# Kernel tuning notes

Measured on AMD Instinct MI355X. Metric: run time of the kernel, lower is better.

Reference implementation:

```python
import jax, jax.numpy as jnp
import numpy as np

EMB = 512
HEADS = 8

def setup_inputs() -> dict:
    key = jax.random.key(0)
    ks = jax.random.split(key, 9)
    s = 1.0 / np.sqrt(EMB)
    return {
        'x':  jax.random.normal(ks[0], (4, 2048, EMB), dtype=jnp.float32),
        'Wq': jax.random.uniform(ks[1], (EMB, EMB), jnp.float32, -s, s),
        'bq': jax.random.uniform(ks[2], (EMB,), jnp.float32, -s, s),
        'Wk': jax.random.uniform(ks[3], (EMB, EMB), jnp.float32, -s, s),
        'bk': jax.random.uniform(ks[4], (EMB,), jnp.float32, -s, s),
        'Wv': jax.random.uniform(ks[5], (EMB, EMB), jnp.float32, -s, s),
        'bv': jax.random.uniform(ks[6], (EMB,), jnp.float32, -s, s),
        'Wo': jax.random.uniform(ks[7], (EMB, EMB), jnp.float32, -s, s),
        'bo': jax.random.uniform(ks[8], (EMB,), jnp.float32, -s, s),
    }

def reference(x, Wq, bq, Wk, bk, Wv, bv, Wo, bo):
    b, n, e = x.shape
    h = HEADS
    d = e // h
    def split_heads(t):
        return t.reshape(b, n, h, d).transpose(0, 2, 1, 3)  # b h n d
    q = split_heads(x @ Wq.T + bq)
    k = split_heads(x @ Wk.T + bk)
    v = split_heads(x @ Wv.T + bv)
    energy = jnp.einsum('bhqd,bhkd->bhqk', q, k)
    scaling = jnp.sqrt(jnp.float32(e))  # NOTE: sqrt(emb_size), not sqrt(head_dim), per source
    att = jax.nn.softmax(energy / scaling, axis=-1)
    out = jnp.einsum('bhal,bhlv->bhav', att, v)  # b h n d
    out = out.transpose(0, 2, 1, 3).reshape(b, n, e)
    return out @ Wo.T + bo
```

## Files before the change

### kernel.cpp

```cpp
#include <hip/hip_runtime.h>

typedef float f32x4 __attribute__((ext_vector_type(4)));
typedef float f32x16 __attribute__((ext_vector_type(16)));
typedef short bf16x8 __attribute__((ext_vector_type(8)));
typedef unsigned int uint;
typedef unsigned short ushort_t;

#define EMB    512
#define NSEQ   2048
#define NBATCH 4
#define NHEAD  8
#define MROWS  (NBATCH * NSEQ)

__device__ __forceinline__ uint f2bf(float x) {
    uint u = __builtin_bit_cast(uint, x);
    return (u + 0x7fffu + ((u >> 16) & 1u)) >> 16;
}

__global__ __launch_bounds__(256)
void prep(const float* __restrict__ x,
          const float* __restrict__ Wq, const float* __restrict__ Wk,
          const float* __restrict__ Wv, const float* __restrict__ Wo,
          const float* __restrict__ bq, const float* __restrict__ bk,
          const float* __restrict__ bv,
          ushort_t* __restrict__ xb, ushort_t* __restrict__ Wqkvb,
          float* __restrict__ bqkv, ushort_t* __restrict__ Wob) {
    int t = blockIdx.x * 256 + threadIdx.x;
    {
        float4 v = ((const float4*)x)[t];
        uint2 p;
        p.x = f2bf(v.x) | (f2bf(v.y) << 16);
        p.y = f2bf(v.z) | (f2bf(v.w) << 16);
        ((uint2*)xb)[t] = p;
    }
    if (t < 65536) {
        float4 a = ((const float4*)Wq)[t];
        float4 b = ((const float4*)Wk)[t];
        float4 c = ((const float4*)Wv)[t];
        float4 d = ((const float4*)Wo)[t];
        uint2 p;
        p.x = f2bf(a.x) | (f2bf(a.y) << 16); p.y = f2bf(a.z) | (f2bf(a.w) << 16);
        ((uint2*)Wqkvb)[t] = p;
        p.x = f2bf(b.x) | (f2bf(b.y) << 16); p.y = f2bf(b.z) | (f2bf(b.w) << 16);
        ((uint2*)Wqkvb)[t + 65536] = p;
        p.x = f2bf(c.x) | (f2bf(c.y) << 16); p.y = f2bf(c.z) | (f2bf(c.w) << 16);
        ((uint2*)Wqkvb)[t + 131072] = p;
        p.x = f2bf(d.x) | (f2bf(d.y) << 16); p.y = f2bf(d.z) | (f2bf(d.w) << 16);
        ((uint2*)Wob)[t] = p;
    }
    if (t < 512) {
        bqkv[t] = bq[t]; bqkv[512 + t] = bk[t]; bqkv[1024 + t] = bv[t];
    }
}

template<int MODE>
__global__ __launch_bounds__(256)
void gemm128(const ushort_t* __restrict__ A, const ushort_t* __restrict__ BT,
             const float* __restrict__ bias, ushort_t* __restrict__ oQK,
             ushort_t* __restrict__ oVT, float* __restrict__ oC) {
    __shared__ ushort_t As[128][40];
    __shared__ ushort_t Bs[128][40];
    const int tid = threadIdx.x, wave = tid >> 6, lane = tid & 63;
    const int m0 = blockIdx.x * 128, n0 = blockIdx.y * 128;
    const int wr = (wave & 1) * 64, wc = (wave >> 1) * 64;

    f32x4 acc[4][4];
#pragma unroll
    for (int i = 0; i < 4; ++i)
#pragma unroll
        for (int j = 0; j < 4; ++j) acc[i][j] = (f32x4){0.f, 0.f, 0.f, 0.f};

    const int sr = tid >> 1, sh = (tid & 1) * 16;
    const ushort_t* Arow = A + (size_t)(m0 + sr) * 512 + sh;
    const ushort_t* Brow = BT + (size_t)(n0 + sr) * 512 + sh;
    const int fr = lane & 15, fc = (lane >> 4) * 8;

    for (int kt = 0; kt < 16; ++kt) {
        uint4 a0 = *(const uint4*)(Arow + kt * 32);
        uint4 a1 = *(const uint4*)(Arow + kt * 32 + 8);
        uint4 b0 = *(const uint4*)(Brow + kt * 32);
        uint4 b1 = *(const uint4*)(Brow + kt * 32 + 8);
        __syncthreads();
        *(uint4*)&As[sr][sh] = a0;  *(uint4*)&As[sr][sh + 8] = a1;
        *(uint4*)&Bs[sr][sh] = b0;  *(uint4*)&Bs[sr][sh + 8] = b1;
        __syncthreads();
        bf16x8 af[4], bf[4];
#pragma unroll
        for (int i = 0; i < 4; ++i) af[i] = *(const bf16x8*)&As[wr + i * 16 + fr][fc];
#pragma unroll
        for (int j = 0; j < 4; ++j) bf[j] = *(const bf16x8*)&Bs[wc + j * 16 + fr][fc];
#pragma unroll
        for (int i = 0; i < 4; ++i)
#pragma unroll
            for (int j = 0; j < 4; ++j)
                acc[i][j] = __builtin_amdgcn_mfma_f32_16x16x32_bf16(af[i], bf[j], acc[i][j], 0, 0, 0);
    }

    const int col_l = lane & 15, row_l = (lane >> 4) * 4;
#pragma unroll
    for (int j = 0; j < 4; ++j) {
        const int col = n0 + wc + j * 16 + col_l;
        const float bv = bias[col];
#pragma unroll
        for (int i = 0; i < 4; ++i) {
            const int row = m0 + wr + i * 16 + row_l;
            f32x4 v = acc[i][j];
            v += (f32x4){bv, bv, bv, bv};
            if (MODE == 0) {
                if (n0 < 1024) {
#pragma unroll
                    for (int r = 0; r < 4; ++r)
                        oQK[(size_t)(row + r) * 1024 + col] = (ushort_t)f2bf(v[r]);
                } else {
                    const int e = col - 1024;
                    const int b = row >> 11, tok = row & 2047;
                    uint2 p;
                    p.x = f2bf(v[0]) | (f2bf(v[1]) << 16);
                    p.y = f2bf(v[2]) | (f2bf(v[3]) << 16);
                    *(uint2*)&oVT[((size_t)(b * 512 + e)) * 2048 + tok] = p;
                }
            } else {
#pragma unroll
                for (int r = 0; r < 4; ++r)
                    oC[(size_t)(row + r) * 512 + col] = v[r];
            }
        }
    }
}

__global__ __launch_bounds__(256)
void attn_mfma(const ushort_t* __restrict__ QK, const ushort_t* __restrict__ VT,
               ushort_t* __restrict__ AO) {
    __shared__ ushort_t Ks[64][72];
    __shared__ ushort_t Vs[64][72];
    __shared__ ushort_t Ps[4][32][72];
    __shared__ float ls[128];

    const int tid = threadIdx.x, w = tid >> 6, lane = tid & 63;
    const int qt = blockIdx.x, bh = blockIdx.y, b = bh >> 3, h = bh & 7;
    const int l31 = lane & 31, lhi = lane >> 5;
    const float cexp = 0.06375872f;

    const size_t qrow = (size_t)(b * NSEQ + qt * 128 + w * 32 + l31);
    bf16x8 qf[4];
#pragma unroll
    for (int ks = 0; ks < 4; ++ks)
        qf[ks] = *(const bf16x8*)&QK[qrow * 1024 + h * 64 + ks * 16 + lhi * 8];

    f32x16 accO[2];
#pragma unroll
    for (int i = 0; i < 16; ++i) { accO[0][i] = 0.f; accO[1][i] = 0.f; }
    float lpart = 0.f;

    const int sr = tid & 63, sc = (tid >> 6) * 16;
    const ushort_t* Kg = QK + (size_t)(b * NSEQ) * 1024 + 512 + h * 64;
    const ushort_t* Vg = VT + ((size_t)(b * 512 + h * 64)) * 2048;

    for (int kt = 0; kt < 32; ++kt) {
        const int k0 = kt * 64;
        uint4 kv0 = *(const uint4*)&Kg[(size_t)(k0 + sr) * 1024 + sc];
        uint4 kv1 = *(const uint4*)&Kg[(size_t)(k0 + sr) * 1024 + sc + 8];
        uint4 vv0 = *(const uint4*)&Vg[(size_t)sr * 2048 + k0 + sc];
        uint4 vv1 = *(const uint4*)&Vg[(size_t)sr * 2048 + k0 + sc + 8];
        __syncthreads();
        *(uint4*)&Ks[sr][sc] = kv0;  *(uint4*)&Ks[sr][sc + 8] = kv1;
        *(uint4*)&Vs[sr][sc] = vv0;  *(uint4*)&Vs[sr][sc + 8] = vv1;
        __syncthreads();

        f32x16 st[2];
#pragma unroll
        for (int i = 0; i < 16; ++i) { st[0][i] = 0.f; st[1][i] = 0.f; }
#pragma unroll
        for (int ks = 0; ks < 4; ++ks) {
            bf16x8 ka0 = *(const bf16x8*)&Ks[l31][ks * 16 + lhi * 8];
            bf16x8 ka1 = *(const bf16x8*)&Ks[32 + l31][ks * 16 + lhi * 8];
            st[0] = __builtin_amdgcn_mfma_f32_32x32x16_bf16(ka0, qf[ks], st[0], 0, 0, 0);
            st[1] = __builtin_amdgcn_mfma_f32_32x32x16_bf16(ka1, qf[ks], st[1], 0, 0, 0);
        }

#pragma unroll
        for (int ms = 0; ms < 2; ++ms) {
#pragma unroll
            for (int g = 0; g < 4; ++g) {
                uint u0 = __builtin_bit_cast(uint, exp2f(st[ms][g * 4 + 0] * cexp));
                uint u1 = __builtin_bit_cast(uint, exp2f(st[ms][g * 4 + 1] * cexp));
                uint u2 = __builtin_bit_cast(uint, exp2f(st[ms][g * 4 + 2] * cexp));
                uint u3 = __builtin_bit_cast(uint, exp2f(st[ms][g * 4 + 3] * cexp));
                lpart += __builtin_bit_cast(float, u0 & 0xffff0000u)
                       + __builtin_bit_cast(float, u1 & 0xffff0000u)
                       + __builtin_bit_cast(float, u2 & 0xffff0000u)
                       + __builtin_bit_cast(float, u3 & 0xffff0000u);
                uint2 p;
                p.x = (u0 >> 16) | (u1 & 0xffff0000u);
                p.y = (u2 >> 16) | (u3 & 0xffff0000u);
                *(uint2*)&Ps[w][l31][ms * 32 + g * 8 + lhi * 4] = p;
            }
        }
        __syncthreads();

#pragma unroll
        for (int ks = 0; ks < 4; ++ks) {
            bf16x8 pa  = *(const bf16x8*)&Ps[w][l31][ks * 16 + lhi * 8];
            bf16x8 vb0 = *(const bf16x8*)&Vs[l31][ks * 16 + lhi * 8];
            bf16x8 vb1 = *(const bf16x8*)&Vs[32 + l31][ks * 16 + lhi * 8];
            accO[0] = __builtin_amdgcn_mfma_f32_32x32x16_bf16(pa, vb0, accO[0], 0, 0, 0);
            accO[1] = __builtin_amdgcn_mfma_f32_32x32x16_bf16(pa, vb1, accO[1], 0, 0, 0);
        }
    }

    float lfull = lpart + __shfl_xor(lpart, 32);
    if (lane < 32) ls[w * 32 + l31] = lfull;
    __syncthreads();

#pragma unroll
    for (int g = 0; g < 4; ++g) {
        float4 lv = *(const float4*)&ls[w * 32 + g * 8 + lhi * 4];
#pragma unroll
        for (int r = 0; r < 4; ++r) {
            const float inv = 1.0f / ((const float*)&lv)[r];
            const int rowp = g * 8 + lhi * 4 + r;
            const size_t orow = (size_t)(b * NSEQ + qt * 128 + w * 32 + rowp);
            AO[orow * 512 + h * 64 + l31]      = (ushort_t)f2bf(accO[0][g * 4 + r] * inv);
            AO[orow * 512 + h * 64 + 32 + l31] = (ushort_t)f2bf(accO[1][g * 4 + r] * inv);
        }
    }
}

extern "C" void kernel_launch(void* const* d_in, const int* in_sizes, int n_in,
                              void* d_out, int out_size, void* d_ws, size_t ws_size,
                              hipStream_t stream) {
    const float* x  = (const float*)d_in[0];
    const float* Wq = (const float*)d_in[1];
    const float* bq = (const float*)d_in[2];
    const float* Wk = (const float*)d_in[3];
    const float* bk = (const float*)d_in[4];
    const float* Wv = (const float*)d_in[5];
    const float* bv = (const float*)d_in[6];
    const float* Wo = (const float*)d_in[7];
    const float* bo = (const float*)d_in[8];

    char* ws = (char*)d_ws;
    ushort_t* xb    = (ushort_t*)(ws);
    ushort_t* Wqkvb = (ushort_t*)(ws + 8388608);
    ushort_t* Wob   = (ushort_t*)(ws + 9961472);
    float*    bqkv  = (float*)   (ws + 10485760);
    ushort_t* QKb   = (ushort_t*)(ws + 10491904);
    ushort_t* VTg   = (ushort_t*)(ws + 27269120);
    ushort_t* AOb   = (ushort_t*)(ws + 35657728);

    prep<<<4096, 256, 0, stream>>>(x, Wq, Wk, Wv, Wo, bq, bk, bv,
                                   xb, Wqkvb, bqkv, Wob);
    gemm128<0><<<dim3(64, 12), 256, 0, stream>>>(xb, Wqkvb, bqkv, QKb, VTg, nullptr);
    attn_mfma<<<dim3(16, 32), 256, 0, stream>>>(QKb, VTg, AOb);
    gemm128<1><<<dim3(64, 4), 256, 0, stream>>>(AOb, Wob, bo, nullptr, nullptr, (float*)d_out);
}
```

Before: 205.1 us.

## Split attention over key range, fold softmax scale into Q, stage GEMM epilogue

The attention kernel gains a template key-slice count. When the workspace is large enough, it runs two slices over halves of the key sequence, writing unnormalized fp32 partial outputs and row sums. A new combine kernel then sums the slices and normalizes. This doubles the number of attention blocks to better fill the GPU, at the cost of extra global traffic and a kernel launch. The softmax scale is now folded into Q in the QKV GEMM epilogue so the raw hardware exp2 can be used, and one per-iteration barrier is dropped. GEMM epilogues are staged through LDS so Q/K and output stores become coalesced vector writes.

```diff
diff --git a/kernel.cpp b/kernel.cpp
--- a/kernel.cpp
+++ b/kernel.cpp
@@ -11,6 +11,7 @@
 #define NBATCH 4
 #define NHEAD  8
 #define MROWS  (NBATCH * NSEQ)
+#define CEXP   0.06375872f
 
 __device__ __forceinline__ uint f2bf(float x) {
     uint u = __builtin_bit_cast(uint, x);
@@ -60,6 +61,7 @@
              ushort_t* __restrict__ oVT, float* __restrict__ oC) {
     __shared__ ushort_t As[128][40];
     __shared__ ushort_t Bs[128][40];
+    __shared__ float ep[32][132];
     const int tid = threadIdx.x, wave = tid >> 6, lane = tid & 63;
     const int m0 = blockIdx.x * 128, n0 = blockIdx.y * 128;
     const int wr = (wave & 1) * 64, wc = (wave >> 1) * 64;
@@ -97,39 +99,76 @@
     }
 
     const int col_l = lane & 15, row_l = (lane >> 4) * 4;
-#pragma unroll
-    for (int j = 0; j < 4; ++j) {
-        const int col = n0 + wc + j * 16 + col_l;
-        const float bv = bias[col];
-#pragma unroll
-        for (int i = 0; i < 4; ++i) {
-            const int row = m0 + wr + i * 16 + row_l;
-            f32x4 v = acc[i][j];
-            v += (f32x4){bv, bv, bv, bv};
-            if (MODE == 0) {
-                if (n0 < 1024) {
+
+    if (MODE == 0 && n0 >= 1024) {
+#pragma unroll
+        for (int j = 0; j < 4; ++j) {
+            const int col = n0 + wc + j * 16 + col_l;
+            const float bv = bias[col];
+#pragma unroll
+            for (int i = 0; i < 4; ++i) {
+                const int row = m0 + wr + i * 16 + row_l;
+                f32x4 v = acc[i][j];
+                v += (f32x4){bv, bv, bv, bv};
+                const int e = col - 1024;
+                const int b = row >> 11, tok = row & 2047;
+                uint2 p;
+                p.x = f2bf(v[0]) | (f2bf(v[1]) << 16);
+                p.y = f2bf(v[2]) | (f2bf(v[3]) << 16);
+                *(uint2*)&oVT[((size_t)(b * 512 + e)) * 2048 + tok] = p;
+            }
+        }
+        return;
+    }
+
+    const float scale = (MODE == 0 && n0 < 512) ? CEXP : 1.0f;
+    float bv[4];
+#pragma unroll
+    for (int j = 0; j < 4; ++j) bv[j] = bias[n0 + wc + j * 16 + col_l];
+
+    const int erow = tid >> 3, eseg = (tid & 7) * 16;
+#pragma unroll
+    for (int c = 0; c < 4; ++c) {
+        __syncthreads();
+        if (wr == (c >> 1) * 64) {
+#pragma unroll
+            for (int ii = 0; ii < 2; ++ii) {
+                const int i = (c & 1) * 2 + ii;
+#pragma unroll
+                for (int j = 0; j < 4; ++j) {
+                    f32x4 v = acc[i][j];
 #pragma unroll
                     for (int r = 0; r < 4; ++r)
-                        oQK[(size_t)(row + r) * 1024 + col] = (ushort_t)f2bf(v[r]);
-                } else {
-                    const int e = col - 1024;
-                    const int b = row >> 11, tok = row & 2047;
-                    uint2 p;
-                    p.x = f2bf(v[0]) | (f2bf(v[1]) << 16);
-                    p.y = f2bf(v[2]) | (f2bf(v[3]) << 16);
-                    *(uint2*)&oVT[((size_t)(b * 512 + e)) * 2048 + tok] = p;
+                        ep[ii * 16 + row_l + r][wc + j * 16 + col_l] = (v[r] + bv[j]) * scale;
                 }
-            } else {
-#pragma unroll
-                for (int r = 0; r < 4; ++r)
-                    oC[(size_t)(row + r) * 512 + col] = v[r];
-            }
-        }
-    }
-}
-
+            }
+        }
+        __syncthreads();
+        const int grow = m0 + c * 32 + erow;
+        if (MODE == 0) {
+            uint4 o0, o1;
+#pragma unroll
+            for (int k = 0; k < 4; ++k) {
+                uint lo = f2bf(ep[erow][eseg + k * 2])     | (f2bf(ep[erow][eseg + k * 2 + 1]) << 16);
+                uint hi = f2bf(ep[erow][eseg + 8 + k * 2]) | (f2bf(ep[erow][eseg + 9 + k * 2]) << 16);
+                ((uint*)&o0)[k] = lo; ((uint*)&o1)[k] = hi;
+            }
+            *(uint4*)&oQK[(size_t)grow * 1024 + n0 + eseg]     = o0;
+            *(uint4*)&oQK[(size_t)grow * 1024 + n0 + eseg + 8] = o1;
+        } else {
+#pragma unroll
+            for (int k = 0; k < 4; ++k) {
+                f32x4 v = *(const f32x4*)&ep[erow][eseg + k * 4];
+                *(f32x4*)&oC[(size_t)grow * 512 + n0 + eseg + k * 4] = v;
+            }
+        }
+    }
+}
+
+template<int NSLICE>
 __global__ __launch_bounds__(256)
 void attn_mfma(const ushort_t* __restrict__ QK, const ushort_t* __restrict__ VT,
+               float* __restrict__ Op, float* __restrict__ Lp,
                ushort_t* __restrict__ AO) {
     __shared__ ushort_t Ks[64][72];
     __shared__ ushort_t Vs[64][72];
@@ -138,8 +177,8 @@
 
     const int tid = threadIdx.x, w = tid >> 6, lane = tid & 63;
     const int qt = blockIdx.x, bh = blockIdx.y, b = bh >> 3, h = bh & 7;
+    const int slice = (NSLICE > 1) ? blockIdx.z : 0;
     const int l31 = lane & 31, lhi = lane >> 5;
-    const float cexp = 0.06375872f;
 
     const size_t qrow = (size_t)(b * NSEQ + qt * 128 + w * 32 + l31);
     bf16x8 qf[4];
@@ -156,7 +195,8 @@
     const ushort_t* Kg = QK + (size_t)(b * NSEQ) * 1024 + 512 + h * 64;
     const ushort_t* Vg = VT + ((size_t)(b * 512 + h * 64)) * 2048;
 
-    for (int kt = 0; kt < 32; ++kt) {
+    const int kt0 = slice * (32 / NSLICE), kt1 = kt0 + 32 / NSLICE;
+    for (int kt = kt0; kt < kt1; ++kt) {
         const int k0 = kt * 64;
         uint4 kv0 = *(const uint4*)&Kg[(size_t)(k0 + sr) * 1024 + sc];
         uint4 kv1 = *(const uint4*)&Kg[(size_t)(k0 + sr) * 1024 + sc + 8];
@@ -182,10 +222,10 @@
         for (int ms = 0; ms < 2; ++ms) {
 #pragma unroll
             for (int g = 0; g < 4; ++g) {
-                uint u0 = __builtin_bit_cast(uint, exp2f(st[ms][g * 4 + 0] * cexp));
-                uint u1 = __builtin_bit_cast(uint, exp2f(st[ms][g * 4 + 1] * cexp));
-                uint u2 = __builtin_bit_cast(uint, exp2f(st[ms][g * 4 + 2] * cexp));
-                uint u3 = __builtin_bit_cast(uint, exp2f(st[ms][g * 4 + 3] * cexp));
+                uint u0 = __builtin_bit_cast(uint, __builtin_amdgcn_exp2f(st[ms][g * 4 + 0]));
+                uint u1 = __builtin_bit_cast(uint, __builtin_amdgcn_exp2f(st[ms][g * 4 + 1]));
+                uint u2 = __builtin_bit_cast(uint, __builtin_amdgcn_exp2f(st[ms][g * 4 + 2]));
+                uint u3 = __builtin_bit_cast(uint, __builtin_amdgcn_exp2f(st[ms][g * 4 + 3]));
                 lpart += __builtin_bit_cast(float, u0 & 0xffff0000u)
                        + __builtin_bit_cast(float, u1 & 0xffff0000u)
                        + __builtin_bit_cast(float, u2 & 0xffff0000u)
@@ -196,7 +236,6 @@
                 *(uint2*)&Ps[w][l31][ms * 32 + g * 8 + lhi * 4] = p;
             }
         }
-        __syncthreads();
 
 #pragma unroll
         for (int ks = 0; ks < 4; ++ks) {
@@ -209,21 +248,53 @@
     }
 
     float lfull = lpart + __shfl_xor(lpart, 32);
-    if (lane < 32) ls[w * 32 + l31] = lfull;
-    __syncthreads();
-
-#pragma unroll
-    for (int g = 0; g < 4; ++g) {
-        float4 lv = *(const float4*)&ls[w * 32 + g * 8 + lhi * 4];
-#pragma unroll
-        for (int r = 0; r < 4; ++r) {
-            const float inv = 1.0f / ((const float*)&lv)[r];
-            const int rowp = g * 8 + lhi * 4 + r;
-            const size_t orow = (size_t)(b * NSEQ + qt * 128 + w * 32 + rowp);
-            AO[orow * 512 + h * 64 + l31]      = (ushort_t)f2bf(accO[0][g * 4 + r] * inv);
-            AO[orow * 512 + h * 64 + 32 + l31] = (ushort_t)f2bf(accO[1][g * 4 + r] * inv);
-        }
-    }
+
+    if (NSLICE == 1) {
+        if (lane < 32) ls[w * 32 + l31] = lfull;
+        __syncthreads();
+#pragma unroll
+        for (int g = 0; g < 4; ++g) {
+            float4 lv = *(const float4*)&ls[w * 32 + g * 8 + lhi * 4];
+#pragma unroll
+            for (int r = 0; r < 4; ++r) {
+                const float inv = 1.0f / ((const float*)&lv)[r];
+                const int rowp = g * 8 + lhi * 4 + r;
+                const size_t orow = (size_t)(b * NSEQ + qt * 128 + w * 32 + rowp);
+                AO[orow * 512 + h * 64 + l31]      = (ushort_t)f2bf(accO[0][g * 4 + r] * inv);
+                AO[orow * 512 + h * 64 + 32 + l31] = (ushort_t)f2bf(accO[1][g * 4 + r] * inv);
+            }
+        }
+    } else {
+        const size_t rowbase = (size_t)(b * NSEQ + qt * 128 + w * 32);
+        if (lane < 32) Lp[(size_t)slice * 65536 + (rowbase + l31) * 8 + h] = lfull;
+        float* Os = Op + (size_t)slice * 4194304;
+#pragma unroll
+        for (int g = 0; g < 4; ++g) {
+#pragma unroll
+            for (int r = 0; r < 4; ++r) {
+                const int rowp = g * 8 + lhi * 4 + r;
+                const size_t orow = rowbase + rowp;
+                Os[orow * 512 + h * 64 + l31]      = accO[0][g * 4 + r];
+                Os[orow * 512 + h * 64 + 32 + l31] = accO[1][g * 4 + r];
+            }
+        }
+    }
+}
+
+__global__ __launch_bounds__(256)
+void combine2(const float* __restrict__ Op, const float* __restrict__ Lp,
+              ushort_t* __restrict__ AO) {
+    const int t = blockIdx.x * 256 + threadIdx.x;
+    const int row = t >> 7;
+    const int c4  = (t & 127) * 4;
+    const int h = c4 >> 6;
+    float4 a = ((const float4*)Op)[t];
+    float4 b = ((const float4*)(Op + 4194304))[t];
+    const float inv = 1.0f / (Lp[row * 8 + h] + Lp[65536 + row * 8 + h]);
+    uint2 p;
+    p.x = f2bf((a.x + b.x) * inv) | (f2bf((a.y + b.y) * inv) << 16);
+    p.y = f2bf((a.z + b.z) * inv) | (f2bf((a.w + b.w) * inv) << 16);
+    ((uint2*)AO)[t] = p;
 }
 
 extern "C" void kernel_launch(void* const* d_in, const int* in_sizes, int n_in,
@@ -247,10 +318,18 @@
     ushort_t* QKb   = (ushort_t*)(ws + 10491904);
     ushort_t* VTg   = (ushort_t*)(ws + 27269120);
     ushort_t* AOb   = (ushort_t*)(ws + 35657728);
+    float*    Opart = (float*)   (ws + 44046336);
+    float*    Lpart = (float*)   (ws + 77600768);
+    const bool split = ws_size >= 78125056;
 
     prep<<<4096, 256, 0, stream>>>(x, Wq, Wk, Wv, Wo, bq, bk, bv,
                                    xb, Wqkvb, bqkv, Wob);
     gemm128<0><<<dim3(64, 12), 256, 0, stream>>>(xb, Wqkvb, bqkv, QKb, VTg, nullptr);
-    attn_mfma<<<dim3(16, 32), 256, 0, stream>>>(QKb, VTg, AOb);
+    if (split) {
+        attn_mfma<2><<<dim3(16, 32, 2), 256, 0, stream>>>(QKb, VTg, Opart, Lpart, nullptr);
+        combine2<<<4096, 256, 0, stream>>>(Opart, Lpart, AOb);
+    } else {
+        attn_mfma<1><<<dim3(16, 32), 256, 0, stream>>>(QKb, VTg, nullptr, nullptr, AOb);
+    }
     gemm128<1><<<dim3(64, 4), 256, 0, stream>>>(AOb, Wob, bo, nullptr, nullptr, (float*)d_out);
 }
```

After: 194.9 us. 5.0% less time.
